# Optimization experiments

Hardware: AMD Instinct MI355X
Metric: run time of the kernel (lower is better)

## Reference

```python
import jax, jax.numpy as jnp
import numpy as np
from itertools import chain, combinations

OBS_DIM = 4096
LAT = 64
NG = 4
GS = OBS_DIM // NG  # 1024 features per group (round-robin i % NG == g)
B = 8192


def _powerset_mask(n):
    subsets = list(chain.from_iterable(combinations(range(n), r) for r in range(1, n + 1)))
    m = np.zeros((len(subsets), n), np.float32)
    for i, s in enumerate(subsets):
        m[i, list(s)] = 1.0
    return jnp.asarray(m)


SUBSET_MASK = _powerset_mask(NG)  # [S, G], S = 2^G - 1 = 15
GROUP_IDX = jnp.asarray(np.stack([np.arange(g, OBS_DIM, NG) for g in range(NG)]), dtype=jnp.int32)  # [G, GS]


def setup_inputs() -> dict:
    key = jax.random.key(0)
    ks = jax.random.split(key, 11)
    s = 0.05
    H = 2 * LAT  # encoder hidden / output width
    return {
        "X": jax.random.normal(ks[0], (B, OBS_DIM), jnp.float32),
        "eps": jax.random.normal(ks[1], (B, LAT), jnp.float32),
        "subset_idx": jax.random.randint(ks[2], (B,), 0, SUBSET_MASK.shape[0], dtype=jnp.int32),
        "enc_w1": jax.random.normal(ks[3], (NG, GS, H), jnp.float32) * s,
        "enc_b1": jnp.zeros((NG, H), jnp.float32),
        "enc_w2": jax.random.normal(ks[4], (NG, H, H), jnp.float32) * s,
        "enc_b2": jnp.zeros((NG, H), jnp.float32),
        "dec_w1": jax.random.normal(ks[5], (NG, LAT, LAT), jnp.float32) * s,
        "dec_b1": jnp.zeros((NG, LAT), jnp.float32),
        "dec_w2": jax.random.normal(ks[6], (NG, LAT, GS), jnp.float32) * s,
        "dec_b2": jnp.zeros((NG, GS), jnp.float32),
    }


def reference(X, eps, subset_idx, enc_w1, enc_b1, enc_w2, enc_b2, dec_w1, dec_b1, dec_w2, dec_b2):
    # ---- encode: per-group gather + tiny MLP (depth=2) ----
    Xg = X[:, GROUP_IDX]  # [B, G, GS] gather of group columns
    h = jax.nn.relu(jnp.einsum('bgi,gih->bgh', Xg, enc_w1) + enc_b1[None])  # [B, G, 2L]
    ml = jnp.einsum('bgh,gho->bgo', h, enc_w2) + enc_b2[None]               # [B, G, 2L]
    means, logvars = jnp.split(ml, 2, axis=-1)  # each [B, G, L]
    means = jnp.transpose(means, (0, 2, 1))     # [B, L, G] (tf stacks groups on axis=2)
    logvars = jnp.transpose(logvars, (0, 2, 1))

    # ---- mopoe: PoE over every non-empty subset of groups ----
    taus = jnp.exp(-logvars)                                   # [B, L, G]
    tau = jnp.einsum('blg,sg->bls', taus, SUBSET_MASK) + 1.0   # [B, L, S] (normalize_outp=True adds 1)
    m_means = jnp.einsum('blg,sg->bls', taus * means, SUBSET_MASK) / tau
    m_logvars = -jnp.log(tau)                                  # log(1/tau)

    # ---- reparameterize: pick one random subset per batch row ----
    sel = subset_idx[:, None, None].astype(jnp.int32)          # [B, 1, 1]
    smean = jnp.take_along_axis(m_means, sel, axis=-1)[..., 0]    # [B, L]
    slogv = jnp.take_along_axis(m_logvars, sel, axis=-1)[..., 0]  # [B, L]
    z = smean + eps * jnp.exp(0.5 * slogv)                     # [B, L]

    # ---- decode: per-group tiny MLP, scatter back to obs_dim ----
    hd = jax.nn.relu(jnp.einsum('bl,glm->bgm', z, dec_w1) + dec_b1[None])  # [B, G, L]
    outg = jnp.einsum('bgm,gmo->bgo', hd, dec_w2) + dec_b2[None]            # [B, G, GS]
    recon = jnp.zeros((X.shape[0], OBS_DIM), X.dtype).at[:, GROUP_IDX.reshape(-1)].set(
        outg.reshape(X.shape[0], -1))
    return recon
```

## Files before the change

### kernel.cpp

```cpp
#include <hip/hip_runtime.h>
#include <hip/hip_bf16.h>
#include <math.h>

#define B_TOT 8192
#define OBS   4096
#define NG    4
#define GSZ   1024
#define LATD  64
#define HDIM  128

typedef __attribute__((ext_vector_type(8))) short   short8_t;
typedef __attribute__((ext_vector_type(8))) unsigned short ushort8_t;
typedef __attribute__((ext_vector_type(4))) float   float4_t;

__constant__ int kMask[15] = {1,2,4,8, 3,5,9,6,10,12, 7,11,13,14, 15};

static __device__ __forceinline__ unsigned short f2b(float x) {
  __hip_bfloat16 b = __float2bfloat16(x);
  return *reinterpret_cast<unsigned short*>(&b);
}
static __device__ __forceinline__ unsigned int pack2(float lo, float hi) {
  return (unsigned int)f2b(lo) | ((unsigned int)f2b(hi) << 16);
}
static __device__ __forceinline__ void gl16(const void* g, void* l) {
  __builtin_amdgcn_global_load_lds(
      (const __attribute__((address_space(1))) void*)g,
      (__attribute__((address_space(3))) void*)l, 16, 0, 0);
}

#define SLOT 1056
#define AQ(row) ((((row) >> 2) * SLOT) + (((row) & 3) * 256))

#define N1 524288
#define N2 65536
#define N3 16384
#define N4 262144
__global__ __launch_bounds__(512) void k_prep0(const float* __restrict__ w1,
                                               const float* __restrict__ w2,
                                               const float* __restrict__ w3,
                                               const float* __restrict__ w4,
                                               const float* __restrict__ X,
                                               unsigned short* __restrict__ W1p,
                                               unsigned short* __restrict__ W2p,
                                               unsigned short* __restrict__ W3p,
                                               unsigned short* __restrict__ W4p,
                                               unsigned short* __restrict__ Xt) {
  const int bx = blockIdx.x;
  if (bx >= 1696) {
    const int t = threadIdx.x;
    const int b = (bx - 1696) * 2 + (t >> 8);
    const int t256 = t & 255;
    const float* p = X + (size_t)b * OBS + t256 * 16;
    const float4_t f0 = *(const float4_t*)(p);
    const float4_t f1 = *(const float4_t*)(p + 4);
    const float4_t f2 = *(const float4_t*)(p + 8);
    const float4_t f3 = *(const float4_t*)(p + 12);
    const int k0 = t256 * 4;
    unsigned short* q = Xt + (size_t)b * OBS;
#pragma unroll
    for (int g = 0; g < 4; ++g) {
      uint2 v;
      v.x = pack2(f0[g], f1[g]);
      v.y = pack2(f2[g], f3[g]);
      *(uint2*)(q + g * GSZ + k0) = v;
    }
    return;
  }
  const int i = bx * 512 + threadIdx.x;
  if (i < N1) {
    const int j = i & 7, oct = (i >> 3) & 3, l15 = (i >> 5) & 15;
    const int ni = (i >> 9) & 1, ks = (i >> 10) & 31;
    const int w = (i >> 15) & 3, g = (i >> 17) & 3;
    const int k = ks * 32 + oct * 8 + j;
    const int h = w * 32 + ni * 16 + l15;
    W1p[i] = f2b(w1[g * 131072 + k * 128 + h]);
  } else if (i < N1 + N2) {
    const int idx = i - N1;
    const int j = idx & 7, oct = (idx >> 3) & 3, l15 = (idx >> 5) & 15;
    const int ni = (idx >> 9) & 7, ks = (idx >> 12) & 3, g = (idx >> 14) & 3;
    const int k = ks * 32 + oct * 8 + j;
    const int col = ni * 16 + l15;
    W2p[idx] = f2b(w2[g * 16384 + k * 128 + col]);
  } else if (i < N1 + N2 + N3) {
    const int idx = i - N1 - N2;
    const int j = idx & 7, oct = (idx >> 3) & 3, l15 = (idx >> 5) & 15;
    const int ni = (idx >> 9) & 3, ks = (idx >> 11) & 1, g = (idx >> 12) & 3;
    const int k = ks * 32 + oct * 8 + j;
    const int m = ni * 16 + l15;
    W3p[idx] = f2b(w3[g * 4096 + k * 64 + m]);
  } else {
    const int idx = i - N1 - N2 - N3;
    const int j = idx & 7, oct = (idx >> 3) & 3, l15 = (idx >> 5) & 15;
    const int ni = (idx >> 9) & 1, ks = (idx >> 10) & 1;
    const int oh = (idx >> 11) & 1, ob = (idx >> 12) & 15, g = (idx >> 16) & 3;
    const int k = ks * 32 + oct * 8 + j;
    const int o = ob * 64 + oh * 32 + ni * 16 + l15;
    W4p[idx] = f2b(w4[g * 65536 + k * 1024 + o]);
  }
}

__global__ __launch_bounds__(512, 2) void k_enc1c(const unsigned short* __restrict__ Xt,
                                                  const unsigned short* __restrict__ W1p,
                                                  const float* __restrict__ B1,
                                                  unsigned short* __restrict__ Hrow) {
  __shared__ __align__(16) char As[2 * 32 * SLOT];

  const int tid = threadIdx.x;
  const int w   = tid >> 6;
  const int l   = tid & 63;
  const int wm  = w & 3;
  const int wn  = w >> 2;
  const int l15 = l & 15;
  const int oct = l >> 4;
  const int rb  = blockIdx.x * 128;
  const int g   = blockIdx.y;
  const int z   = blockIdx.z;
  const int lofs = (l15 * 4 + oct) * 8;

  const unsigned short* const xsrc =
      Xt + (size_t)(rb + (l >> 4)) * OBS + g * GSZ + (l & 15) * 8;

#pragma unroll
  for (int i = 0; i < 4; ++i) {
    const int s = i * 8 + w;
    gl16(xsrc + (size_t)(s * 4) * OBS, As + s * SLOT);
  }
  __syncthreads();

  float4_t acc[2][2];
#pragma unroll
  for (int i = 0; i < 2; ++i)
#pragma unroll
    for (int j = 0; j < 2; ++j) acc[i][j] = (float4_t){0.f, 0.f, 0.f, 0.f};

  const int cw = z * 2 + wn;
  const unsigned short* const bbase = W1p + (size_t)(g * 4 + cw) * 32768 + lofs;

  for (int c = 0; c < 8; ++c) {
    const int cur = c & 1;
    if (c < 7) {
#pragma unroll
      for (int i = 0; i < 4; ++i) {
        const int s = i * 8 + w;
        gl16(xsrc + (size_t)(s * 4) * OBS + (c + 1) * 128,
             As + (cur ^ 1) * 32 * SLOT + s * SLOT);
      }
    }
#pragma unroll
    for (int ks = 0; ks < 4; ++ks) {
      const int ksg = c * 4 + ks;
      short8_t af[2], bf[2];
#pragma unroll
      for (int mi = 0; mi < 2; ++mi)
        af[mi] = *(const short8_t*)(As + cur * 32 * SLOT +
                                    AQ(wm * 32 + mi * 16 + l15) +
                                    ks * 64 + oct * 16);
#pragma unroll
      for (int ni = 0; ni < 2; ++ni)
        bf[ni] = *(const short8_t*)(bbase + (size_t)ksg * 1024 + ni * 512);
#pragma unroll
      for (int mi = 0; mi < 2; ++mi)
#pragma unroll
        for (int ni = 0; ni < 2; ++ni)
          acc[mi][ni] = __builtin_amdgcn_mfma_f32_16x16x32_bf16(af[mi], bf[ni], acc[mi][ni], 0, 0, 0);
    }
    __syncthreads();
  }

  unsigned short* const ob = (unsigned short*)As;
#pragma unroll
  for (int ni = 0; ni < 2; ++ni) {
    const int c32  = ni * 16 + l15;
    const int gcol = g * 128 + z * 64 + wn * 32 + c32;
    const float b  = B1[gcol];
#pragma unroll
    for (int mi = 0; mi < 2; ++mi)
#pragma unroll
      for (int j = 0; j < 4; ++j)
        ob[(wm * 32 + mi * 16 + oct * 4 + j) * 72 + wn * 32 + c32] =
            f2b(fmaxf(acc[mi][ni][j] + b, 0.0f));
  }
  __syncthreads();

  {
    const int row = tid >> 2, seg = tid & 3;
    unsigned short* dst = Hrow + (size_t)(rb + row) * 512 + g * 128 + z * 64 + seg * 16;
    const unsigned short* src = &ob[row * 72 + seg * 16];
    *(ushort8_t*)(dst)     = *(const ushort8_t*)(src);
    *(ushort8_t*)(dst + 8) = *(const ushort8_t*)(src + 8);
  }
}

__global__ __launch_bounds__(256, 4) void k_samp4(const unsigned short* __restrict__ Hrow,
                                                  const unsigned short* __restrict__ W2p,
                                                  const unsigned short* __restrict__ W3p,
                                                  const float* __restrict__ B2,
                                                  const float* __restrict__ DB1,
                                                  const float* __restrict__ eps,
                                                  const int*   __restrict__ subset_idx,
                                                  unsigned short* __restrict__ Hd) {
  __shared__ __align__(16) float mls[16 * 516];
  __shared__ __align__(16) unsigned short zbp[2 * 512];

  const int tid = threadIdx.x;
  const int g   = tid >> 6;
  const int l   = tid & 63;
  const int l15 = l & 15;
  const int oct = l >> 4;
  const int rb  = blockIdx.x * 16;
  const int lofs = (l15 * 4 + oct) * 8;

  float4_t acc[8];
#pragma unroll
  for (int j = 0; j < 8; ++j) acc[j] = (float4_t){0.f, 0.f, 0.f, 0.f};
  {
    const unsigned short* arow = Hrow + (size_t)(rb + l15) * 512 + g * 128 + oct * 8;
    const unsigned short* bb   = W2p + (size_t)g * 16384 + lofs;
#pragma unroll
    for (int ks = 0; ks < 4; ++ks) {
      const short8_t af = *(const short8_t*)(arow + ks * 32);
#pragma unroll
      for (int ni = 0; ni < 8; ++ni) {
        const short8_t bf = *(const short8_t*)(bb + ks * 4096 + ni * 512);
        acc[ni] = __builtin_amdgcn_mfma_f32_16x16x32_bf16(af, bf, acc[ni], 0, 0, 0);
      }
    }
  }

#pragma unroll
  for (int ni = 0; ni < 8; ++ni) {
    const int col = g * 128 + ni * 16 + l15;
    const float b = B2[col];
#pragma unroll
    for (int j = 0; j < 4; ++j)
      mls[(oct * 4 + j) * 516 + col] = acc[ni][j] + b;
  }
  __syncthreads();

#pragma unroll
  for (int qq = 0; qq < 4; ++qq) {
    const int idx = qq * 256 + tid;
    const int r   = idx >> 6;
    const int ll  = idx & 63;
    const int m   = kMask[subset_idx[rb + r]];
    float tau = 1.0f, num = 0.0f;
#pragma unroll
    for (int gg = 0; gg < 4; ++gg) {
      if (m & (1 << gg)) {
        const float lv = mls[r * 516 + gg * 128 + 64 + ll];
        const float mu = mls[r * 516 + gg * 128 + ll];
        const float t  = expf(-lv);
        tau += t;
        num = fmaf(t, mu, num);
      }
    }
    const float zv = num / tau + eps[(size_t)(rb + r) * LATD + ll] * rsqrtf(tau);
    zbp[(ll >> 5) * 512 + (r * 4 + ((ll >> 3) & 3)) * 8 + (ll & 7)] = f2b(zv);
  }
  __syncthreads();

  float4_t a3[4];
#pragma unroll
  for (int j = 0; j < 4; ++j) a3[j] = (float4_t){0.f, 0.f, 0.f, 0.f};
  {
    const unsigned short* bb = W3p + (size_t)g * 4096 + lofs;
#pragma unroll
    for (int ks = 0; ks < 2; ++ks) {
      const short8_t af = *(const short8_t*)&zbp[ks * 512 + lofs];
#pragma unroll
      for (int ni = 0; ni < 4; ++ni) {
        const short8_t bf = *(const short8_t*)(bb + ks * 2048 + ni * 512);
        a3[ni] = __builtin_amdgcn_mfma_f32_16x16x32_bf16(af, bf, a3[ni], 0, 0, 0);
      }
    }
  }
#pragma unroll
  for (int ni = 0; ni < 4; ++ni) {
    const int col = g * 64 + ni * 16 + l15;
    const float b = DB1[col];
#pragma unroll
    for (int j = 0; j < 4; ++j)
      Hd[(size_t)(rb + oct * 4 + j) * 256 + col] = f2b(fmaxf(a3[ni][j] + b, 0.0f));
  }
}

__global__ __launch_bounds__(512) void k_dec2(const unsigned short* __restrict__ Hd,
                                              const unsigned short* __restrict__ W4p,
                                              const float* __restrict__ Bb,
                                              float* __restrict__ Out) {
  __shared__ float obuf[32][264];

  const int tid = threadIdx.x;
  const int w   = tid >> 6;
  const int l   = tid & 63;
  const int g   = w >> 1;
  const int oh  = w & 1;
  const int r0  = blockIdx.x * 32;
  const int ob  = blockIdx.y * 64;
  const int l15 = l & 15;
  const int oct = l >> 4;
  const int lofs = (l15 * 4 + oct) * 8;

  float4_t acc[2][2];
#pragma unroll
  for (int i = 0; i < 2; ++i)
#pragma unroll
    for (int j = 0; j < 2; ++j) acc[i][j] = (float4_t){0.f, 0.f, 0.f, 0.f};

  const unsigned short* bb4 = W4p + ((g * 16 + blockIdx.y) * 2 + oh) * 2048 + lofs;

#pragma unroll
  for (int ks = 0; ks < 2; ++ks) {
    short8_t af[2], bf[2];
#pragma unroll
    for (int mi = 0; mi < 2; ++mi)
      af[mi] = *(const short8_t*)(Hd + (size_t)(r0 + mi * 16 + l15) * 256 +
                                  g * 64 + ks * 32 + oct * 8);
#pragma unroll
    for (int ni = 0; ni < 2; ++ni)
      bf[ni] = *(const short8_t*)(bb4 + ks * 1024 + ni * 512);
#pragma unroll
    for (int mi = 0; mi < 2; ++mi)
#pragma unroll
      for (int ni = 0; ni < 2; ++ni)
        acc[mi][ni] = __builtin_amdgcn_mfma_f32_16x16x32_bf16(af[mi], bf[ni], acc[mi][ni], 0, 0, 0);
  }

#pragma unroll
  for (int ni = 0; ni < 2; ++ni) {
    const int lo = oh * 32 + ni * 16 + l15;
    const float b = Bb[g * 1024 + ob + lo];
#pragma unroll
    for (int mi = 0; mi < 2; ++mi) {
      const int rloc = mi * 16 + oct * 4;
#pragma unroll
      for (int j = 0; j < 4; ++j)
        obuf[rloc + j][4 * lo + g] = acc[mi][ni][j] + b;
    }
  }
  __syncthreads();

#pragma unroll
  for (int i = 0; i < 4; ++i) {
    const int q = tid + i * 512;
    const int row = q >> 6, c4 = q & 63;
    const float4 v = *(const float4*)&obuf[row][c4 * 4];
    *(float4*)(Out + (size_t)(r0 + row) * OBS + 4 * ob + c4 * 4) = v;
  }
}

extern "C" void kernel_launch(void* const* d_in, const int* in_sizes, int n_in,
                              void* d_out, int out_size, void* d_ws, size_t ws_size,
                              hipStream_t stream) {
  const float* X          = (const float*)d_in[0];
  const float* eps        = (const float*)d_in[1];
  const int*   subset_idx = (const int*)  d_in[2];
  const float* enc_w1     = (const float*)d_in[3];
  const float* enc_b1     = (const float*)d_in[4];
  const float* enc_w2     = (const float*)d_in[5];
  const float* enc_b2     = (const float*)d_in[6];
  const float* dec_w1     = (const float*)d_in[7];
  const float* dec_b1     = (const float*)d_in[8];
  const float* dec_w2     = (const float*)d_in[9];
  const float* dec_b2     = (const float*)d_in[10];
  float* out = (float*)d_out;

  char* wsb = (char*)d_ws;
  unsigned short* Xt   = (unsigned short*)wsb;
  unsigned short* Hrow = (unsigned short*)(wsb + (64u << 20));
  unsigned short* Hd   = (unsigned short*)(wsb + (72u << 20));
  unsigned short* W1p  = (unsigned short*)(wsb + (76u << 20));
  unsigned short* W2p  = (unsigned short*)(wsb + (77u << 20));
  unsigned short* W3p  = (unsigned short*)(wsb + (77u << 20) + (128u << 10));
  unsigned short* W4p  = (unsigned short*)(wsb + (77u << 20) + (160u << 10));

  k_prep0<<<5792, 512, 0, stream>>>(enc_w1, enc_w2, dec_w1, dec_w2, X,
                                    W1p, W2p, W3p, W4p, Xt);
  k_enc1c<<<dim3(64, 4, 2), 512, 0, stream>>>(Xt, W1p, enc_b1, Hrow);
  k_samp4<<<512, 256, 0, stream>>>(Hrow, W2p, W3p, enc_b2, dec_b1,
                                   eps, subset_idx, Hd);
  k_dec2<<<dim3(256, 16), 512, 0, stream>>>(Hd, W4p, dec_b2, out);
}
```

Baseline: 129.2 us.

## Retile encoder GEMM, split second encoder layer from PoE sampling kernel

The first encoder kernel now has each block cover 64 rows and all 128 output columns of a group, without the z split, so each X tile is read once instead of twice. The second encoder layer moves into its own kernel with a wider grid, writing fp32 means and logvars to a workspace buffer. A separate PoE kernel stages W3 in shared memory and runs the decoder's first layer. This adds a kernel launch and an fp32 round trip through global memory in exchange for more parallelism and less redundant X traffic.

```diff
diff --git a/kernel.cpp b/kernel.cpp
--- a/kernel.cpp
+++ b/kernel.cpp
@@ -99,11 +99,11 @@
   }
 }
 
-__global__ __launch_bounds__(512, 2) void k_enc1c(const unsigned short* __restrict__ Xt,
+__global__ __launch_bounds__(512, 4) void k_enc1e(const unsigned short* __restrict__ Xt,
                                                   const unsigned short* __restrict__ W1p,
                                                   const float* __restrict__ B1,
                                                   unsigned short* __restrict__ Hrow) {
-  __shared__ __align__(16) char As[2 * 32 * SLOT];
+  __shared__ __align__(16) char As[2 * 16 * SLOT];
 
   const int tid = threadIdx.x;
   const int w   = tid >> 6;
@@ -112,128 +112,162 @@
   const int wn  = w >> 2;
   const int l15 = l & 15;
   const int oct = l >> 4;
-  const int rb  = blockIdx.x * 128;
+  const int rb  = blockIdx.x * 64;
   const int g   = blockIdx.y;
-  const int z   = blockIdx.z;
   const int lofs = (l15 * 4 + oct) * 8;
 
   const unsigned short* const xsrc =
       Xt + (size_t)(rb + (l >> 4)) * OBS + g * GSZ + (l & 15) * 8;
 
 #pragma unroll
-  for (int i = 0; i < 4; ++i) {
+  for (int i = 0; i < 2; ++i) {
     const int s = i * 8 + w;
     gl16(xsrc + (size_t)(s * 4) * OBS, As + s * SLOT);
   }
   __syncthreads();
 
-  float4_t acc[2][2];
-#pragma unroll
-  for (int i = 0; i < 2; ++i)
-#pragma unroll
-    for (int j = 0; j < 2; ++j) acc[i][j] = (float4_t){0.f, 0.f, 0.f, 0.f};
-
-  const int cw = z * 2 + wn;
-  const unsigned short* const bbase = W1p + (size_t)(g * 4 + cw) * 32768 + lofs;
+  float4_t acc[4];
+#pragma unroll
+  for (int j = 0; j < 4; ++j) acc[j] = (float4_t){0.f, 0.f, 0.f, 0.f};
+
+  const unsigned short* const bbase = W1p + (size_t)(g * 4) * 32768 + lofs;
 
   for (int c = 0; c < 8; ++c) {
     const int cur = c & 1;
     if (c < 7) {
 #pragma unroll
-      for (int i = 0; i < 4; ++i) {
+      for (int i = 0; i < 2; ++i) {
         const int s = i * 8 + w;
         gl16(xsrc + (size_t)(s * 4) * OBS + (c + 1) * 128,
-             As + (cur ^ 1) * 32 * SLOT + s * SLOT);
+             As + (cur ^ 1) * 16 * SLOT + s * SLOT);
       }
     }
 #pragma unroll
     for (int ks = 0; ks < 4; ++ks) {
       const int ksg = c * 4 + ks;
-      short8_t af[2], bf[2];
-#pragma unroll
-      for (int mi = 0; mi < 2; ++mi)
-        af[mi] = *(const short8_t*)(As + cur * 32 * SLOT +
-                                    AQ(wm * 32 + mi * 16 + l15) +
-                                    ks * 64 + oct * 16);
-#pragma unroll
-      for (int ni = 0; ni < 2; ++ni)
-        bf[ni] = *(const short8_t*)(bbase + (size_t)ksg * 1024 + ni * 512);
-#pragma unroll
-      for (int mi = 0; mi < 2; ++mi)
-#pragma unroll
-        for (int ni = 0; ni < 2; ++ni)
-          acc[mi][ni] = __builtin_amdgcn_mfma_f32_16x16x32_bf16(af[mi], bf[ni], acc[mi][ni], 0, 0, 0);
+      const short8_t af = *(const short8_t*)(As + cur * 16 * SLOT +
+                                             AQ(wm * 16 + l15) +
+                                             ks * 64 + oct * 16);
+      short8_t bf[4];
+#pragma unroll
+      for (int ni = 0; ni < 4; ++ni)
+        bf[ni] = *(const short8_t*)(bbase + (size_t)(wn * 2 + (ni >> 1)) * 32768 +
+                                    (size_t)ksg * 1024 + (ni & 1) * 512);
+#pragma unroll
+      for (int ni = 0; ni < 4; ++ni)
+        acc[ni] = __builtin_amdgcn_mfma_f32_16x16x32_bf16(af, bf[ni], acc[ni], 0, 0, 0);
     }
     __syncthreads();
   }
 
   unsigned short* const ob = (unsigned short*)As;
 #pragma unroll
-  for (int ni = 0; ni < 2; ++ni) {
-    const int c32  = ni * 16 + l15;
-    const int gcol = g * 128 + z * 64 + wn * 32 + c32;
-    const float b  = B1[gcol];
-#pragma unroll
-    for (int mi = 0; mi < 2; ++mi)
-#pragma unroll
-      for (int j = 0; j < 4; ++j)
-        ob[(wm * 32 + mi * 16 + oct * 4 + j) * 72 + wn * 32 + c32] =
-            f2b(fmaxf(acc[mi][ni][j] + b, 0.0f));
-  }
-  __syncthreads();
-
+  for (int ni = 0; ni < 4; ++ni) {
+    const int c128 = wn * 64 + ni * 16 + l15;
+    const float b  = B1[g * 128 + c128];
+#pragma unroll
+    for (int j = 0; j < 4; ++j)
+      ob[(wm * 16 + oct * 4 + j) * 136 + c128] = f2b(fmaxf(acc[ni][j] + b, 0.0f));
+  }
+  __syncthreads();
   {
-    const int row = tid >> 2, seg = tid & 3;
-    unsigned short* dst = Hrow + (size_t)(rb + row) * 512 + g * 128 + z * 64 + seg * 16;
-    const unsigned short* src = &ob[row * 72 + seg * 16];
+    const int row = tid >> 3, seg = tid & 7;
+    unsigned short* dst = Hrow + (size_t)(rb + row) * 512 + g * 128 + seg * 16;
+    const unsigned short* src = &ob[row * 136 + seg * 16];
     *(ushort8_t*)(dst)     = *(const ushort8_t*)(src);
     *(ushort8_t*)(dst + 8) = *(const ushort8_t*)(src + 8);
   }
 }
 
-__global__ __launch_bounds__(256, 4) void k_samp4(const unsigned short* __restrict__ Hrow,
-                                                  const unsigned short* __restrict__ W2p,
-                                                  const unsigned short* __restrict__ W3p,
-                                                  const float* __restrict__ B2,
-                                                  const float* __restrict__ DB1,
-                                                  const float* __restrict__ eps,
-                                                  const int*   __restrict__ subset_idx,
-                                                  unsigned short* __restrict__ Hd) {
-  __shared__ __align__(16) float mls[16 * 516];
-  __shared__ __align__(16) unsigned short zbp[2 * 512];
+__global__ __launch_bounds__(256) void k_enc2d(const unsigned short* __restrict__ Hrow,
+                                               const unsigned short* __restrict__ W2p,
+                                               const float* __restrict__ B2,
+                                               float* __restrict__ Mlg) {
+  __shared__ __align__(16) float obuf[32 * 132];
 
   const int tid = threadIdx.x;
-  const int g   = tid >> 6;
+  const int cq  = tid >> 6;
+  const int l   = tid & 63;
+  const int l15 = l & 15;
+  const int oct = l >> 4;
+  const int rb  = blockIdx.x * 32;
+  const int g   = blockIdx.y;
+  const int lofs = (l15 * 4 + oct) * 8;
+
+  float4_t acc[2][2];
+#pragma unroll
+  for (int i = 0; i < 2; ++i)
+#pragma unroll
+    for (int j = 0; j < 2; ++j) acc[i][j] = (float4_t){0.f, 0.f, 0.f, 0.f};
+
+  const unsigned short* const bb = W2p + (size_t)g * 16384 + lofs;
+
+#pragma unroll
+  for (int ks = 0; ks < 4; ++ks) {
+    short8_t af[2], bf[2];
+#pragma unroll
+    for (int mi = 0; mi < 2; ++mi)
+      af[mi] = *(const short8_t*)(Hrow + (size_t)(rb + mi * 16 + l15) * 512 +
+                                  g * 128 + ks * 32 + oct * 8);
+#pragma unroll
+    for (int ni = 0; ni < 2; ++ni)
+      bf[ni] = *(const short8_t*)(bb + ks * 4096 + (cq * 2 + ni) * 512);
+#pragma unroll
+    for (int mi = 0; mi < 2; ++mi)
+#pragma unroll
+      for (int ni = 0; ni < 2; ++ni)
+        acc[mi][ni] = __builtin_amdgcn_mfma_f32_16x16x32_bf16(af[mi], bf[ni], acc[mi][ni], 0, 0, 0);
+  }
+
+#pragma unroll
+  for (int ni = 0; ni < 2; ++ni) {
+    const int c128 = cq * 32 + ni * 16 + l15;
+    const float b = B2[g * 128 + c128];
+#pragma unroll
+    for (int mi = 0; mi < 2; ++mi)
+#pragma unroll
+      for (int j = 0; j < 4; ++j)
+        obuf[(mi * 16 + oct * 4 + j) * 132 + c128] = acc[mi][ni][j] + b;
+  }
+  __syncthreads();
+
+  {
+    const int row = tid >> 3, seg = tid & 7;
+    float* dst = Mlg + (size_t)(rb + row) * 512 + g * 128 + seg * 16;
+    const float* src = &obuf[row * 132 + seg * 16];
+#pragma unroll
+    for (int i = 0; i < 4; ++i)
+      *(float4*)(dst + i * 4) = *(const float4*)(src + i * 4);
+  }
+}
+
+__global__ __launch_bounds__(256, 2) void k_poe(const float* __restrict__ Mlg,
+                                                const unsigned short* __restrict__ W3p,
+                                                const float* __restrict__ DB1,
+                                                const float* __restrict__ eps,
+                                                const int*   __restrict__ subset_idx,
+                                                unsigned short* __restrict__ Hd) {
+  __shared__ __align__(16) float mls16[16 * 516];
+  __shared__ __align__(16) unsigned short zbs[16 * 72];
+  __shared__ __align__(16) char lW3[32768];
+
+  const int tid = threadIdx.x;
+  const int w   = tid >> 6;
   const int l   = tid & 63;
   const int l15 = l & 15;
   const int oct = l >> 4;
   const int rb  = blockIdx.x * 16;
-  const int lofs = (l15 * 4 + oct) * 8;
-
-  float4_t acc[8];
-#pragma unroll
-  for (int j = 0; j < 8; ++j) acc[j] = (float4_t){0.f, 0.f, 0.f, 0.f};
+  const int lofs = (l15 * 4 + oct) * 16;
+
+#pragma unroll
+  for (int i = 0; i < 8; ++i)
+    gl16((const char*)W3p + (w * 8 + i) * 1024 + l * 16, lW3 + (w * 8 + i) * 1024);
   {
-    const unsigned short* arow = Hrow + (size_t)(rb + l15) * 512 + g * 128 + oct * 8;
-    const unsigned short* bb   = W2p + (size_t)g * 16384 + lofs;
-#pragma unroll
-    for (int ks = 0; ks < 4; ++ks) {
-      const short8_t af = *(const short8_t*)(arow + ks * 32);
-#pragma unroll
-      for (int ni = 0; ni < 8; ++ni) {
-        const short8_t bf = *(const short8_t*)(bb + ks * 4096 + ni * 512);
-        acc[ni] = __builtin_amdgcn_mfma_f32_16x16x32_bf16(af, bf, acc[ni], 0, 0, 0);
-      }
-    }
-  }
-
-#pragma unroll
-  for (int ni = 0; ni < 8; ++ni) {
-    const int col = g * 128 + ni * 16 + l15;
-    const float b = B2[col];
-#pragma unroll
-    for (int j = 0; j < 4; ++j)
-      mls[(oct * 4 + j) * 516 + col] = acc[ni][j] + b;
+    const int row = tid >> 4, c0 = (tid & 15) * 32;
+    const float* src = Mlg + (size_t)(rb + row) * 512 + c0;
+#pragma unroll
+    for (int i = 0; i < 8; ++i)
+      *(float4*)&mls16[row * 516 + c0 + i * 4] = *(const float4*)(src + i * 4);
   }
   __syncthreads();
 
@@ -247,36 +281,35 @@
 #pragma unroll
     for (int gg = 0; gg < 4; ++gg) {
       if (m & (1 << gg)) {
-        const float lv = mls[r * 516 + gg * 128 + 64 + ll];
-        const float mu = mls[r * 516 + gg * 128 + ll];
+        const float lv = mls16[r * 516 + gg * 128 + 64 + ll];
+        const float mu = mls16[r * 516 + gg * 128 + ll];
         const float t  = expf(-lv);
         tau += t;
         num = fmaf(t, mu, num);
       }
     }
     const float zv = num / tau + eps[(size_t)(rb + r) * LATD + ll] * rsqrtf(tau);
-    zbp[(ll >> 5) * 512 + (r * 4 + ((ll >> 3) & 3)) * 8 + (ll & 7)] = f2b(zv);
+    zbs[r * 72 + ll] = f2b(zv);
   }
   __syncthreads();
 
   float4_t a3[4];
 #pragma unroll
   for (int j = 0; j < 4; ++j) a3[j] = (float4_t){0.f, 0.f, 0.f, 0.f};
-  {
-    const unsigned short* bb = W3p + (size_t)g * 4096 + lofs;
-#pragma unroll
-    for (int ks = 0; ks < 2; ++ks) {
-      const short8_t af = *(const short8_t*)&zbp[ks * 512 + lofs];
-#pragma unroll
-      for (int ni = 0; ni < 4; ++ni) {
-        const short8_t bf = *(const short8_t*)(bb + ks * 2048 + ni * 512);
-        a3[ni] = __builtin_amdgcn_mfma_f32_16x16x32_bf16(af, bf, a3[ni], 0, 0, 0);
-      }
+#pragma unroll
+  for (int ks = 0; ks < 2; ++ks) {
+    const short8_t af = *(const short8_t*)((const char*)zbs +
+                        (l15 * 72 + ks * 32 + oct * 8) * 2);
+#pragma unroll
+    for (int ni = 0; ni < 4; ++ni) {
+      const short8_t bf = *(const short8_t*)(lW3 + w * 8192 + ks * 4096 +
+                                             ni * 1024 + lofs);
+      a3[ni] = __builtin_amdgcn_mfma_f32_16x16x32_bf16(af, bf, a3[ni], 0, 0, 0);
     }
   }
 #pragma unroll
   for (int ni = 0; ni < 4; ++ni) {
-    const int col = g * 64 + ni * 16 + l15;
+    const int col = w * 64 + ni * 16 + l15;
     const float b = DB1[col];
 #pragma unroll
     for (int j = 0; j < 4; ++j)
@@ -368,16 +401,17 @@
   char* wsb = (char*)d_ws;
   unsigned short* Xt   = (unsigned short*)wsb;
   unsigned short* Hrow = (unsigned short*)(wsb + (64u << 20));
-  unsigned short* Hd   = (unsigned short*)(wsb + (72u << 20));
-  unsigned short* W1p  = (unsigned short*)(wsb + (76u << 20));
-  unsigned short* W2p  = (unsigned short*)(wsb + (77u << 20));
-  unsigned short* W3p  = (unsigned short*)(wsb + (77u << 20) + (128u << 10));
-  unsigned short* W4p  = (unsigned short*)(wsb + (77u << 20) + (160u << 10));
+  float*          Mlg  = (float*)(wsb + (72u << 20));
+  unsigned short* Hd   = (unsigned short*)(wsb + (88u << 20));
+  unsigned short* W1p  = (unsigned short*)(wsb + (92u << 20));
+  unsigned short* W2p  = (unsigned short*)(wsb + (93u << 20));
+  unsigned short* W3p  = (unsigned short*)(wsb + (93u << 20) + (128u << 10));
+  unsigned short* W4p  = (unsigned short*)(wsb + (93u << 20) + (160u << 10));
 
   k_prep0<<<5792, 512, 0, stream>>>(enc_w1, enc_w2, dec_w1, dec_w2, X,
                                     W1p, W2p, W3p, W4p, Xt);
-  k_enc1c<<<dim3(64, 4, 2), 512, 0, stream>>>(Xt, W1p, enc_b1, Hrow);
-  k_samp4<<<512, 256, 0, stream>>>(Hrow, W2p, W3p, enc_b2, dec_b1,
-                                   eps, subset_idx, Hd);
+  k_enc1e<<<dim3(128, 4), 512, 0, stream>>>(Xt, W1p, enc_b1, Hrow);
+  k_enc2d<<<dim3(256, 4), 256, 0, stream>>>(Hrow, W2p, enc_b2, Mlg);
+  k_poe<<<512, 256, 0, stream>>>(Mlg, W3p, dec_b1, eps, subset_idx, Hd);
   k_dec2<<<dim3(256, 16), 512, 0, stream>>>(Hd, W4p, dec_b2, out);
 }
```

Measured after the change: 154.2 us. 19.3% more time.
